# Kernel tuning notes

Measured on AMD Instinct MI355X. Metric: run time of the kernel, lower is better.

The kernel has to match this reference:

```python
import jax, jax.numpy as jnp
import numpy as np

B, N, D = 2048, 64, 256
DH = D // 2  # theta/phi projection dim
EPS = 1e-5

def layer_norm(x, g, b):
    m = jnp.mean(x, axis=-1, keepdims=True)
    v = jnp.var(x, axis=-1, keepdims=True)
    return (x - m) * jax.lax.rsqrt(v + EPS) * g + b

def graph_conv(x, adj, th_w, ph_w, fc_w, fc_b):
    # static adjacency: softmax over rows, shared across batch
    A_static = jax.nn.softmax(adj, axis=-1)  # [N, N]
    q = jnp.einsum('bnd,hd->bnh', x, th_w)   # [B, N, DH]
    k = jnp.einsum('bnd,hd->bnh', x, ph_w)   # [B, N, DH]
    scores = jnp.einsum('bni,bmi->bnm', q, k) / jnp.sqrt(jnp.asarray(DH, x.dtype))
    A_hat = A_static[None] + jax.nn.softmax(scores, axis=-1)  # [B, N, N]
    agg = jnp.einsum('bnm,bmd->bnd', A_hat, x)
    return jnp.einsum('bnd,od->bno', agg, fc_w) + fc_b

def setup_inputs() -> dict:
    key = jax.random.key(0)
    ks = jax.random.split(key, 12)
    eye = jnp.eye(N, dtype=jnp.float32)
    s = 1.0 / np.sqrt(D)
    return {
        'graph':  jax.random.normal(ks[0], (B, N, D), jnp.float32),
        'ln_in_g': jnp.ones((D,), jnp.float32), 'ln_in_b': jnp.zeros((D,), jnp.float32),
        'adj0':  eye + 0.01 * jax.random.normal(ks[1], (N, N), jnp.float32),
        'th0':   jax.random.uniform(ks[2], (DH, D), jnp.float32, -s, s),
        'ph0':   jax.random.uniform(ks[3], (DH, D), jnp.float32, -s, s),
        'fcw0':  jax.random.uniform(ks[4], (D, D), jnp.float32, -s, s),
        'fcb0':  jax.random.uniform(ks[5], (D,), jnp.float32, -s, s),
        'ln0_g': jnp.ones((D,), jnp.float32), 'ln0_b': jnp.zeros((D,), jnp.float32),
        'adj1':  eye + 0.01 * jax.random.normal(ks[6], (N, N), jnp.float32),
        'th1':   jax.random.uniform(ks[7], (DH, D), jnp.float32, -s, s),
        'ph1':   jax.random.uniform(ks[8], (DH, D), jnp.float32, -s, s),
        'fcw1':  jax.random.uniform(ks[9], (D, D), jnp.float32, -s, s),
        'fcb1':  jax.random.uniform(ks[10], (D,), jnp.float32, -s, s),
    }

def reference(graph, ln_in_g, ln_in_b, adj0, th0, ph0, fcw0, fcb0,
              ln0_g, ln0_b, adj1, th1, ph1, fcw1, fcb1):
    x = layer_norm(graph, ln_in_g, ln_in_b)
    x = graph_conv(x, adj0, th0, ph0, fcw0, fcb0)
    x = layer_norm(x, ln0_g, ln0_b)
    x = jnp.where(x >= 0, x, 0.1 * x)  # LeakyReLU(0.1); dropout is identity in eval
    x = graph_conv(x, adj1, th1, ph1, fcw1, fcb1)
    return x
```

## Files before the change

kernel.cpp:

```cpp
#include <hip/hip_runtime.h>

typedef __bf16 bf16x8 __attribute__((ext_vector_type(8)));
typedef __bf16 bf16x4 __attribute__((ext_vector_type(4)));
typedef float  f32x4  __attribute__((ext_vector_type(4)));

constexpr int WS_AS0 = 0;
constexpr int WS_AS1 = 4096;
constexpr int WS_MT0 = 8192;
constexpr int WS_MT1 = 73728;
constexpr int WS_FC0 = 139264;
constexpr int WS_FC1 = 204800;

static __device__ __forceinline__ f32x4 mfma16(bf16x8 a, bf16x8 b, f32x4 c) {
    return __builtin_amdgcn_mfma_f32_16x16x32_bf16(a, b, c, 0, 0, 0);
}

__global__ void prep_all(const float* __restrict__ adj0, const float* __restrict__ adj1,
                         const float* __restrict__ th0,  const float* __restrict__ ph0,
                         const float* __restrict__ th1,  const float* __restrict__ ph1,
                         const float* __restrict__ fc0,  const float* __restrict__ fc1,
                         __bf16* __restrict__ wsb) {
    const int blk = blockIdx.x, tid = threadIdx.x;
    if (blk < 32) {
        const int w = tid >> 6, lane = tid & 63;
        const int row = blk * 4 + w;
        const int layer = row >> 6, r = row & 63;
        const float* a = (layer ? adj1 : adj0) + r * 64;
        const float v = a[lane];
        float mx = v;
        #pragma unroll
        for (int m = 1; m < 64; m <<= 1) mx = fmaxf(mx, __shfl_xor(mx, m));
        float e = __expf(v - mx), sum = e;
        #pragma unroll
        for (int m = 1; m < 64; m <<= 1) sum += __shfl_xor(sum, m);
        wsb[(layer ? WS_AS1 : WS_AS0) + r * 64 + lane] = (__bf16)(e / sum);
    } else if (blk < 544) {
        const int e = (blk - 32) & 255, layer = (blk - 32) >> 8, d = tid;
        const float* th = layer ? th1 : th0;
        const float* ph = layer ? ph1 : ph0;
        float s = 0.f;
        #pragma unroll 8
        for (int h = 0; h < 128; ++h) s += ph[h * 256 + e] * th[h * 256 + d];
        wsb[(layer ? WS_MT1 : WS_MT0) + e * 256 + d] = (__bf16)(s * 0.088388347648318447f);
    } else {
        const int i = (blk - 544) * 512 + tid * 2;
        if (i < 65536) {
            wsb[WS_FC0 + i]     = (__bf16)fc0[i];
            wsb[WS_FC0 + i + 1] = (__bf16)fc0[i + 1];
        } else {
            wsb[WS_FC1 + i - 65536] = (__bf16)fc1[i - 65536];
            wsb[WS_FC1 + i - 65535] = (__bf16)fc1[i - 65535];
        }
    }
}

__global__ __launch_bounds__(512, 4) void fused_gcn(
    const float* __restrict__ graph,
    const float* __restrict__ ln_in_g, const float* __restrict__ ln_in_b,
    const __bf16* __restrict__ wsb,
    const float* __restrict__ fcb0, const float* __restrict__ ln0_g,
    const float* __restrict__ ln0_b, const float* __restrict__ fcb1,
    float* __restrict__ outp)
{
    constexpr int XN_S = 264;
    constexpr int ZT_S = 72;
    constexpr int AH_S = 72;

    __shared__ __align__(16) __bf16 sXn[64 * XN_S];
    __shared__ __align__(16) __bf16 sR1[256 * ZT_S];
    __shared__ __align__(16) __bf16 sAh[64 * AH_S];
    __shared__ float sRed[128];

    const int tid = threadIdx.x;
    const int w = tid >> 6, lane = tid & 63;
    const int l15 = lane & 15, qd = lane >> 4;
    const int b = blockIdx.x;

    {
        if (tid < 128) sRed[tid] = 0.f;
        const int r = tid >> 3, ci = (tid & 7) * 32;
        const float* gp = graph + (size_t)b * 16384 + r * 256 + ci;
        f32x4 v[8];
        float s = 0.f, s2 = 0.f;
        #pragma unroll
        for (int j = 0; j < 8; ++j) {
            v[j] = *(const f32x4*)(gp + j * 4);
            #pragma unroll
            for (int e = 0; e < 4; ++e) { s += v[j][e]; s2 += v[j][e] * v[j][e]; }
        }
        #pragma unroll
        for (int m = 1; m <= 4; m <<= 1) { s += __shfl_xor(s, m); s2 += __shfl_xor(s2, m); }
        const float mean = s * (1.f / 256.f);
        const float var  = s2 * (1.f / 256.f) - mean * mean;
        const float rstd = rsqrtf(var + 1e-5f);
        #pragma unroll
        for (int j = 0; j < 8; ++j) {
            f32x4 gg = *(const f32x4*)(ln_in_g + ci + j * 4);
            f32x4 bb = *(const f32x4*)(ln_in_b + ci + j * 4);
            bf16x4 pk;
            #pragma unroll
            for (int e = 0; e < 4; ++e)
                pk[e] = (__bf16)((v[j][e] - mean) * rstd * gg[e] + bb[e]);
            *(bf16x4*)&sXn[r * XN_S + ci + j * 4] = pk;
        }
    }
    __syncthreads();

    #pragma unroll 1
    for (int layer = 0; layer < 2; ++layer) {
        const __bf16* As  = wsb + (layer ? WS_AS1 : WS_AS0);
        const __bf16* mtw = wsb + (layer ? WS_MT1 : WS_MT0);
        const __bf16* fcw = wsb + (layer ? WS_FC1 : WS_FC0);
        const float*  fcb = layer ? fcb1 : fcb0;

        {
            {
                const int r = tid >> 3, c8 = (tid & 7) * 8;
                *(bf16x8*)&sAh[r * AH_S + c8] = *(const bf16x8*)(As + r * 64 + c8);
            }
            #pragma unroll
            for (int jm = 0; jm < 2; ++jm) {
                bf16x8 amt[8];
                #pragma unroll
                for (int kk = 0; kk < 8; ++kk)
                    amt[kk] = *(const bf16x8*)(mtw + ((w * 2 + jm) * 16 + l15) * 256 + kk * 32 + qd * 8);
                f32x4 tacc[4];
                #pragma unroll
                for (int nt = 0; nt < 4; ++nt) tacc[nt] = (f32x4){0.f, 0.f, 0.f, 0.f};
                #pragma unroll
                for (int kk = 0; kk < 8; ++kk)
                    #pragma unroll
                    for (int nt = 0; nt < 4; ++nt) {
                        bf16x8 bx = *(const bf16x8*)&sXn[(nt * 16 + l15) * XN_S + kk * 32 + qd * 8];
                        tacc[nt] = mfma16(amt[kk], bx, tacc[nt]);
                    }
                #pragma unroll
                for (int nt = 0; nt < 4; ++nt) {
                    bf16x4 pk;
                    #pragma unroll
                    for (int r = 0; r < 4; ++r) pk[r] = (__bf16)tacc[nt][r];
                    *(bf16x4*)&sR1[(nt * 16 + l15) * XN_S + (w * 2 + jm) * 16 + qd * 4] = pk;
                }
            }
        }
        __syncthreads();

        if (w < 4) {
            const int mb = w * 16;
            bf16x8 at[8];
            #pragma unroll
            for (int kk = 0; kk < 8; ++kk)
                at[kk] = *(const bf16x8*)&sR1[(mb + l15) * XN_S + kk * 32 + qd * 8];
            f32x4 sc[4];
            #pragma unroll
            for (int nt = 0; nt < 4; ++nt) sc[nt] = (f32x4){0.f, 0.f, 0.f, 0.f};
            #pragma unroll
            for (int nt = 0; nt < 4; ++nt)
                #pragma unroll
                for (int kk = 0; kk < 8; ++kk) {
                    bf16x8 bx = *(const bf16x8*)&sXn[(nt * 16 + l15) * XN_S + kk * 32 + qd * 8];
                    sc[nt] = mfma16(at[kk], bx, sc[nt]);
                }
            #pragma unroll
            for (int r = 0; r < 4; ++r) {
                float v[4];
                #pragma unroll
                for (int nt = 0; nt < 4; ++nt) v[nt] = sc[nt][r];
                float mx = fmaxf(fmaxf(v[0], v[1]), fmaxf(v[2], v[3]));
                #pragma unroll
                for (int m = 1; m <= 8; m <<= 1) mx = fmaxf(mx, __shfl_xor(mx, m));
                float e[4], sum = 0.f;
                #pragma unroll
                for (int nt = 0; nt < 4; ++nt) { e[nt] = __expf(v[nt] - mx); sum += e[nt]; }
                #pragma unroll
                for (int m = 1; m <= 8; m <<= 1) sum += __shfl_xor(sum, m);
                const float inv = 1.f / sum;
                const int row = mb + qd * 4 + r;
                #pragma unroll
                for (int nt = 0; nt < 4; ++nt) {
                    const int col = nt * 16 + l15;
                    const float as = (float)sAh[row * AH_S + col];
                    sAh[row * AH_S + col] = (__bf16)(e[nt] * inv + as);
                }
            }
        }
        __syncthreads();

        {
            #pragma unroll
            for (int jm = 0; jm < 2; ++jm) {
                const int o = w * 32 + jm * 16 + l15;
                bf16x8 bfc[8];
                #pragma unroll
                for (int kk = 0; kk < 8; ++kk)
                    bfc[kk] = *(const bf16x8*)(fcw + o * 256 + kk * 32 + qd * 8);
                f32x4 zacc[4];
                #pragma unroll
                for (int m = 0; m < 4; ++m) zacc[m] = (f32x4){0.f, 0.f, 0.f, 0.f};
                #pragma unroll
                for (int kk = 0; kk < 8; ++kk)
                    #pragma unroll
                    for (int m = 0; m < 4; ++m) {
                        bf16x8 ax = *(const bf16x8*)&sXn[(m * 16 + l15) * XN_S + kk * 32 + qd * 8];
                        zacc[m] = mfma16(ax, bfc[kk], zacc[m]);
                    }
                #pragma unroll
                for (int m = 0; m < 4; ++m) {
                    bf16x4 pk;
                    #pragma unroll
                    for (int r = 0; r < 4; ++r) pk[r] = (__bf16)zacc[m][r];
                    *(bf16x4*)&sR1[o * ZT_S + m * 16 + qd * 4] = pk;
                }
            }
        }
        __syncthreads();

        {
            const int mb = (w & 3) * 16, ng = w >> 2;
            bf16x8 aa[2];
            #pragma unroll
            for (int kk = 0; kk < 2; ++kk)
                aa[kk] = *(const bf16x8*)&sAh[(mb + l15) * AH_S + kk * 32 + qd * 8];
            f32x4 oacc[8];
            #pragma unroll
            for (int j = 0; j < 8; ++j) {
                const int o = ng * 128 + j * 16 + l15;
                f32x4 acc = {0.f, 0.f, 0.f, 0.f};
                #pragma unroll
                for (int kk = 0; kk < 2; ++kk) {
                    bf16x8 bb = *(const bf16x8*)&sR1[o * ZT_S + kk * 32 + qd * 8];
                    acc = mfma16(aa[kk], bb, acc);
                }
                const float bias = fcb[o];
                #pragma unroll
                for (int r = 0; r < 4; ++r) acc[r] += bias;
                oacc[j] = acc;
            }

            if (layer == 0) {
                #pragma unroll
                for (int r = 0; r < 4; ++r) {
                    float s = 0.f, s2 = 0.f;
                    #pragma unroll
                    for (int j = 0; j < 8; ++j) { const float vv = oacc[j][r]; s += vv; s2 += vv * vv; }
                    #pragma unroll
                    for (int m = 1; m <= 8; m <<= 1) { s += __shfl_xor(s, m); s2 += __shfl_xor(s2, m); }
                    if (l15 == 0) {
                        const int row = mb + qd * 4 + r;
                        atomicAdd(&sRed[row], s);
                        atomicAdd(&sRed[64 + row], s2);
                    }
                }
                __syncthreads();
                float mean4[4], rstd4[4];
                #pragma unroll
                for (int r = 0; r < 4; ++r) {
                    const int row = mb + qd * 4 + r;
                    const float mean = sRed[row] * (1.f / 256.f);
                    const float var  = sRed[64 + row] * (1.f / 256.f) - mean * mean;
                    mean4[r] = mean;
                    rstd4[r] = rsqrtf(var + 1e-5f);
                }
                #pragma unroll
                for (int j = 0; j < 8; ++j) {
                    const int o = ng * 128 + j * 16 + l15;
                    const float g = ln0_g[o], bb = ln0_b[o];
                    #pragma unroll
                    for (int r = 0; r < 4; ++r) {
                        float y = (oacc[j][r] - mean4[r]) * rstd4[r] * g + bb;
                        y = (y >= 0.f) ? y : 0.1f * y;
                        sXn[(mb + qd * 4 + r) * XN_S + o] = (__bf16)y;
                    }
                }
                __syncthreads();
            } else {
                float* op = outp + (size_t)b * 16384;
                #pragma unroll
                for (int j = 0; j < 8; ++j) {
                    const int o = ng * 128 + j * 16 + l15;
                    #pragma unroll
                    for (int r = 0; r < 4; ++r)
                        op[(mb + qd * 4 + r) * 256 + o] = oacc[j][r];
                }
            }
        }
    }
}

extern "C" void kernel_launch(void* const* d_in, const int* in_sizes, int n_in,
                              void* d_out, int out_size, void* d_ws, size_t ws_size,
                              hipStream_t stream) {
    const float* graph   = (const float*)d_in[0];
    const float* ln_in_g = (const float*)d_in[1];
    const float* ln_in_b = (const float*)d_in[2];
    const float* adj0    = (const float*)d_in[3];
    const float* th0     = (const float*)d_in[4];
    const float* ph0     = (const float*)d_in[5];
    const float* fcw0    = (const float*)d_in[6];
    const float* fcb0    = (const float*)d_in[7];
    const float* ln0_g   = (const float*)d_in[8];
    const float* ln0_b   = (const float*)d_in[9];
    const float* adj1    = (const float*)d_in[10];
    const float* th1     = (const float*)d_in[11];
    const float* ph1     = (const float*)d_in[12];
    const float* fcw1    = (const float*)d_in[13];
    const float* fcb1    = (const float*)d_in[14];
    __bf16* wsb = (__bf16*)d_ws;

    prep_all<<<800, 256, 0, stream>>>(adj0, adj1, th0, ph0, th1, ph1, fcw0, fcw1, wsb);
    fused_gcn<<<2048, 512, 0, stream>>>(graph, ln_in_g, ln_in_b, wsb,
                                        fcb0, ln0_g, ln0_b, fcb1, (float*)d_out);
}
```

Measured before the change: 404.4 us.

## Persistent blocks over four batches with graph prefetch and fused theta/fc GEMM

The grid shrinks from 2048 to 512 blocks, and each block loops over four batch elements. The next batch's graph rows are prefetched into registers during the second layer, so the global load overlaps compute. The theta projection and fc projection GEMMs are merged into one pass over sXn. The fc result is held in registers and written to shared memory after the softmax phase, which removes one barrier phase. The costs are higher register pressure (the prefetch buffer plus zpk) and fewer blocks, which may leave compute units underused on a 256-CU GPU.

```diff
diff --git a/kernel.cpp b/kernel.cpp
--- a/kernel.cpp
+++ b/kernel.cpp
@@ -74,213 +74,219 @@
     const int tid = threadIdx.x;
     const int w = tid >> 6, lane = tid & 63;
     const int l15 = lane & 15, qd = lane >> 4;
-    const int b = blockIdx.x;
-
+    const int r8 = tid >> 3, ci8 = (tid & 7) * 32;
+
+    f32x4 gv[8];
     {
-        if (tid < 128) sRed[tid] = 0.f;
-        const int r = tid >> 3, ci = (tid & 7) * 32;
-        const float* gp = graph + (size_t)b * 16384 + r * 256 + ci;
-        f32x4 v[8];
-        float s = 0.f, s2 = 0.f;
+        const float* gp = graph + (size_t)blockIdx.x * 16384 + r8 * 256 + ci8;
         #pragma unroll
-        for (int j = 0; j < 8; ++j) {
-            v[j] = *(const f32x4*)(gp + j * 4);
+        for (int j = 0; j < 8; ++j) gv[j] = *(const f32x4*)(gp + j * 4);
+    }
+
+    #pragma unroll 1
+    for (int it = 0; it < 4; ++it) {
+        const int b = blockIdx.x + it * 512;
+
+        {
+            if (tid < 128) sRed[tid] = 0.f;
+            float s = 0.f, s2 = 0.f;
             #pragma unroll
-            for (int e = 0; e < 4; ++e) { s += v[j][e]; s2 += v[j][e] * v[j][e]; }
-        }
-        #pragma unroll
-        for (int m = 1; m <= 4; m <<= 1) { s += __shfl_xor(s, m); s2 += __shfl_xor(s2, m); }
-        const float mean = s * (1.f / 256.f);
-        const float var  = s2 * (1.f / 256.f) - mean * mean;
-        const float rstd = rsqrtf(var + 1e-5f);
-        #pragma unroll
-        for (int j = 0; j < 8; ++j) {
-            f32x4 gg = *(const f32x4*)(ln_in_g + ci + j * 4);
-            f32x4 bb = *(const f32x4*)(ln_in_b + ci + j * 4);
-            bf16x4 pk;
+            for (int j = 0; j < 8; ++j)
+                #pragma unroll
+                for (int e = 0; e < 4; ++e) { s += gv[j][e]; s2 += gv[j][e] * gv[j][e]; }
             #pragma unroll
-            for (int e = 0; e < 4; ++e)
-                pk[e] = (__bf16)((v[j][e] - mean) * rstd * gg[e] + bb[e]);
-            *(bf16x4*)&sXn[r * XN_S + ci + j * 4] = pk;
-        }
-    }
-    __syncthreads();
-
-    #pragma unroll 1
-    for (int layer = 0; layer < 2; ++layer) {
-        const __bf16* As  = wsb + (layer ? WS_AS1 : WS_AS0);
-        const __bf16* mtw = wsb + (layer ? WS_MT1 : WS_MT0);
-        const __bf16* fcw = wsb + (layer ? WS_FC1 : WS_FC0);
-        const float*  fcb = layer ? fcb1 : fcb0;
-
-        {
-            {
-                const int r = tid >> 3, c8 = (tid & 7) * 8;
-                *(bf16x8*)&sAh[r * AH_S + c8] = *(const bf16x8*)(As + r * 64 + c8);
-            }
+            for (int m = 1; m <= 4; m <<= 1) { s += __shfl_xor(s, m); s2 += __shfl_xor(s2, m); }
+            const float mean = s * (1.f / 256.f);
+            const float var  = s2 * (1.f / 256.f) - mean * mean;
+            const float rstd = rsqrtf(var + 1e-5f);
             #pragma unroll
-            for (int jm = 0; jm < 2; ++jm) {
-                bf16x8 amt[8];
-                #pragma unroll
-                for (int kk = 0; kk < 8; ++kk)
-                    amt[kk] = *(const bf16x8*)(mtw + ((w * 2 + jm) * 16 + l15) * 256 + kk * 32 + qd * 8);
-                f32x4 tacc[4];
-                #pragma unroll
-                for (int nt = 0; nt < 4; ++nt) tacc[nt] = (f32x4){0.f, 0.f, 0.f, 0.f};
-                #pragma unroll
-                for (int kk = 0; kk < 8; ++kk)
-                    #pragma unroll
-                    for (int nt = 0; nt < 4; ++nt) {
-                        bf16x8 bx = *(const bf16x8*)&sXn[(nt * 16 + l15) * XN_S + kk * 32 + qd * 8];
-                        tacc[nt] = mfma16(amt[kk], bx, tacc[nt]);
-                    }
-                #pragma unroll
-                for (int nt = 0; nt < 4; ++nt) {
-                    bf16x4 pk;
-                    #pragma unroll
-                    for (int r = 0; r < 4; ++r) pk[r] = (__bf16)tacc[nt][r];
-                    *(bf16x4*)&sR1[(nt * 16 + l15) * XN_S + (w * 2 + jm) * 16 + qd * 4] = pk;
-                }
+            for (int j = 0; j < 8; ++j) {
+                f32x4 gg = *(const f32x4*)(ln_in_g + ci8 + j * 4);
+                f32x4 bb = *(const f32x4*)(ln_in_b + ci8 + j * 4);
+                bf16x4 pk;
+                #pragma unroll
+                for (int e = 0; e < 4; ++e)
+                    pk[e] = (__bf16)((gv[j][e] - mean) * rstd * gg[e] + bb[e]);
+                *(bf16x4*)&sXn[r8 * XN_S + ci8 + j * 4] = pk;
             }
         }
         __syncthreads();
 
-        if (w < 4) {
-            const int mb = w * 16;
-            bf16x8 at[8];
-            #pragma unroll
-            for (int kk = 0; kk < 8; ++kk)
-                at[kk] = *(const bf16x8*)&sR1[(mb + l15) * XN_S + kk * 32 + qd * 8];
-            f32x4 sc[4];
-            #pragma unroll
-            for (int nt = 0; nt < 4; ++nt) sc[nt] = (f32x4){0.f, 0.f, 0.f, 0.f};
-            #pragma unroll
-            for (int nt = 0; nt < 4; ++nt)
-                #pragma unroll
-                for (int kk = 0; kk < 8; ++kk) {
-                    bf16x8 bx = *(const bf16x8*)&sXn[(nt * 16 + l15) * XN_S + kk * 32 + qd * 8];
-                    sc[nt] = mfma16(at[kk], bx, sc[nt]);
-                }
-            #pragma unroll
-            for (int r = 0; r < 4; ++r) {
-                float v[4];
-                #pragma unroll
-                for (int nt = 0; nt < 4; ++nt) v[nt] = sc[nt][r];
-                float mx = fmaxf(fmaxf(v[0], v[1]), fmaxf(v[2], v[3]));
-                #pragma unroll
-                for (int m = 1; m <= 8; m <<= 1) mx = fmaxf(mx, __shfl_xor(mx, m));
-                float e[4], sum = 0.f;
-                #pragma unroll
-                for (int nt = 0; nt < 4; ++nt) { e[nt] = __expf(v[nt] - mx); sum += e[nt]; }
-                #pragma unroll
-                for (int m = 1; m <= 8; m <<= 1) sum += __shfl_xor(sum, m);
-                const float inv = 1.f / sum;
-                const int row = mb + qd * 4 + r;
-                #pragma unroll
-                for (int nt = 0; nt < 4; ++nt) {
-                    const int col = nt * 16 + l15;
-                    const float as = (float)sAh[row * AH_S + col];
-                    sAh[row * AH_S + col] = (__bf16)(e[nt] * inv + as);
-                }
-            }
-        }
-        __syncthreads();
-
-        {
-            #pragma unroll
-            for (int jm = 0; jm < 2; ++jm) {
-                const int o = w * 32 + jm * 16 + l15;
-                bf16x8 bfc[8];
+        #pragma unroll 1
+        for (int layer = 0; layer < 2; ++layer) {
+            const __bf16* As  = wsb + (layer ? WS_AS1 : WS_AS0);
+            const __bf16* mtw = wsb + (layer ? WS_MT1 : WS_MT0);
+            const __bf16* fcw = wsb + (layer ? WS_FC1 : WS_FC0);
+            const float*  fcb = layer ? fcb1 : fcb0;
+
+            bf16x4 zpk[4][2];
+
+            {
+                {
+                    const int rr = tid >> 3, c8 = (tid & 7) * 8;
+                    *(bf16x8*)&sAh[rr * AH_S + c8] = *(const bf16x8*)(As + rr * 64 + c8);
+                }
+                #pragma unroll
+                for (int jm = 0; jm < 2; ++jm) {
+                    const int row = w * 32 + jm * 16 + l15;
+                    f32x4 tacc[4], zacc[4];
+                    #pragma unroll
+                    for (int i = 0; i < 4; ++i) {
+                        tacc[i] = (f32x4){0.f, 0.f, 0.f, 0.f};
+                        zacc[i] = (f32x4){0.f, 0.f, 0.f, 0.f};
+                    }
+                    #pragma unroll
+                    for (int kk = 0; kk < 8; ++kk) {
+                        const int co = kk * 32 + qd * 8;
+                        bf16x8 amt = *(const bf16x8*)(mtw + row * 256 + co);
+                        bf16x8 afc = *(const bf16x8*)(fcw + row * 256 + co);
+                        #pragma unroll
+                        for (int nt = 0; nt < 4; ++nt) {
+                            bf16x8 bx = *(const bf16x8*)&sXn[(nt * 16 + l15) * XN_S + co];
+                            tacc[nt] = mfma16(amt, bx, tacc[nt]);
+                            zacc[nt] = mfma16(bx, afc, zacc[nt]);
+                        }
+                    }
+                    #pragma unroll
+                    for (int nt = 0; nt < 4; ++nt) {
+                        bf16x4 pk;
+                        #pragma unroll
+                        for (int r = 0; r < 4; ++r) pk[r] = (__bf16)tacc[nt][r];
+                        *(bf16x4*)&sR1[(nt * 16 + l15) * XN_S + (w * 2 + jm) * 16 + qd * 4] = pk;
+                    }
+                    #pragma unroll
+                    for (int nt = 0; nt < 4; ++nt)
+                        #pragma unroll
+                        for (int r = 0; r < 4; ++r)
+                            zpk[nt][jm][r] = (__bf16)zacc[nt][r];
+                }
+            }
+            __syncthreads();
+
+            if (w < 4) {
+                const int mb = w * 16;
+                bf16x8 at[8];
                 #pragma unroll
                 for (int kk = 0; kk < 8; ++kk)
-                    bfc[kk] = *(const bf16x8*)(fcw + o * 256 + kk * 32 + qd * 8);
-                f32x4 zacc[4];
-                #pragma unroll
-                for (int m = 0; m < 4; ++m) zacc[m] = (f32x4){0.f, 0.f, 0.f, 0.f};
-                #pragma unroll
-                for (int kk = 0; kk < 8; ++kk)
-                    #pragma unroll
-                    for (int m = 0; m < 4; ++m) {
-                        bf16x8 ax = *(const bf16x8*)&sXn[(m * 16 + l15) * XN_S + kk * 32 + qd * 8];
-                        zacc[m] = mfma16(ax, bfc[kk], zacc[m]);
-                    }
-                #pragma unroll
-                for (int m = 0; m < 4; ++m) {
-                    bf16x4 pk;
-                    #pragma unroll
-                    for (int r = 0; r < 4; ++r) pk[r] = (__bf16)zacc[m][r];
-                    *(bf16x4*)&sR1[o * ZT_S + m * 16 + qd * 4] = pk;
-                }
-            }
-        }
-        __syncthreads();
-
-        {
-            const int mb = (w & 3) * 16, ng = w >> 2;
-            bf16x8 aa[2];
-            #pragma unroll
-            for (int kk = 0; kk < 2; ++kk)
-                aa[kk] = *(const bf16x8*)&sAh[(mb + l15) * AH_S + kk * 32 + qd * 8];
-            f32x4 oacc[8];
-            #pragma unroll
-            for (int j = 0; j < 8; ++j) {
-                const int o = ng * 128 + j * 16 + l15;
-                f32x4 acc = {0.f, 0.f, 0.f, 0.f};
-                #pragma unroll
-                for (int kk = 0; kk < 2; ++kk) {
-                    bf16x8 bb = *(const bf16x8*)&sR1[o * ZT_S + kk * 32 + qd * 8];
-                    acc = mfma16(aa[kk], bb, acc);
-                }
-                const float bias = fcb[o];
-                #pragma unroll
-                for (int r = 0; r < 4; ++r) acc[r] += bias;
-                oacc[j] = acc;
-            }
-
-            if (layer == 0) {
+                    at[kk] = *(const bf16x8*)&sR1[(mb + l15) * XN_S + kk * 32 + qd * 8];
+                f32x4 sc[4];
+                #pragma unroll
+                for (int nt = 0; nt < 4; ++nt) sc[nt] = (f32x4){0.f, 0.f, 0.f, 0.f};
+                #pragma unroll
+                for (int nt = 0; nt < 4; ++nt)
+                    #pragma unroll
+                    for (int kk = 0; kk < 8; ++kk) {
+                        bf16x8 bx = *(const bf16x8*)&sXn[(nt * 16 + l15) * XN_S + kk * 32 + qd * 8];
+                        sc[nt] = mfma16(at[kk], bx, sc[nt]);
+                    }
                 #pragma unroll
                 for (int r = 0; r < 4; ++r) {
-                    float s = 0.f, s2 = 0.f;
-                    #pragma unroll
-                    for (int j = 0; j < 8; ++j) { const float vv = oacc[j][r]; s += vv; s2 += vv * vv; }
-                    #pragma unroll
-                    for (int m = 1; m <= 8; m <<= 1) { s += __shfl_xor(s, m); s2 += __shfl_xor(s2, m); }
-                    if (l15 == 0) {
-                        const int row = mb + qd * 4 + r;
-                        atomicAdd(&sRed[row], s);
-                        atomicAdd(&sRed[64 + row], s2);
-                    }
-                }
-                __syncthreads();
-                float mean4[4], rstd4[4];
-                #pragma unroll
-                for (int r = 0; r < 4; ++r) {
+                    float v[4];
+                    #pragma unroll
+                    for (int nt = 0; nt < 4; ++nt) v[nt] = sc[nt][r];
+                    float mx = fmaxf(fmaxf(v[0], v[1]), fmaxf(v[2], v[3]));
+                    #pragma unroll
+                    for (int m = 1; m <= 8; m <<= 1) mx = fmaxf(mx, __shfl_xor(mx, m));
+                    float e[4], sum = 0.f;
+                    #pragma unroll
+                    for (int nt = 0; nt < 4; ++nt) { e[nt] = __expf(v[nt] - mx); sum += e[nt]; }
+                    #pragma unroll
+                    for (int m = 1; m <= 8; m <<= 1) sum += __shfl_xor(sum, m);
+                    const float inv = 1.f / sum;
                     const int row = mb + qd * 4 + r;
-                    const float mean = sRed[row] * (1.f / 256.f);
-                    const float var  = sRed[64 + row] * (1.f / 256.f) - mean * mean;
-                    mean4[r] = mean;
-                    rstd4[r] = rsqrtf(var + 1e-5f);
-                }
+                    #pragma unroll
+                    for (int nt = 0; nt < 4; ++nt) {
+                        const int col = nt * 16 + l15;
+                        const float as = (float)sAh[row * AH_S + col];
+                        sAh[row * AH_S + col] = (__bf16)(e[nt] * inv + as);
+                    }
+                }
+            }
+            __syncthreads();
+
+            {
+                #pragma unroll
+                for (int jm = 0; jm < 2; ++jm) {
+                    const int o = w * 32 + jm * 16 + l15;
+                    #pragma unroll
+                    for (int nt = 0; nt < 4; ++nt)
+                        *(bf16x4*)&sR1[o * ZT_S + nt * 16 + qd * 4] = zpk[nt][jm];
+                }
+            }
+            if (layer == 1 && it < 3) {
+                const float* gp = graph + (size_t)(b + 512) * 16384 + r8 * 256 + ci8;
+                #pragma unroll
+                for (int j = 0; j < 8; ++j) gv[j] = *(const f32x4*)(gp + j * 4);
+            }
+            __syncthreads();
+
+            {
+                const int mb = (w & 3) * 16, ng = w >> 2;
+                bf16x8 aa[2];
+                #pragma unroll
+                for (int kk = 0; kk < 2; ++kk)
+                    aa[kk] = *(const bf16x8*)&sAh[(mb + l15) * AH_S + kk * 32 + qd * 8];
+                f32x4 oacc[8];
                 #pragma unroll
                 for (int j = 0; j < 8; ++j) {
                     const int o = ng * 128 + j * 16 + l15;
-                    const float g = ln0_g[o], bb = ln0_b[o];
+                    f32x4 acc = {0.f, 0.f, 0.f, 0.f};
+                    #pragma unroll
+                    for (int kk = 0; kk < 2; ++kk) {
+                        bf16x8 bb = *(const bf16x8*)&sR1[o * ZT_S + kk * 32 + qd * 8];
+                        acc = mfma16(aa[kk], bb, acc);
+                    }
+                    const float bias = fcb[o];
+                    #pragma unroll
+                    for (int r = 0; r < 4; ++r) acc[r] += bias;
+                    oacc[j] = acc;
+                }
+
+                if (layer == 0) {
                     #pragma unroll
                     for (int r = 0; r < 4; ++r) {
-                        float y = (oacc[j][r] - mean4[r]) * rstd4[r] * g + bb;
-                        y = (y >= 0.f) ? y : 0.1f * y;
-                        sXn[(mb + qd * 4 + r) * XN_S + o] = (__bf16)y;
-                    }
-                }
-                __syncthreads();
-            } else {
-                float* op = outp + (size_t)b * 16384;
-                #pragma unroll
-                for (int j = 0; j < 8; ++j) {
-                    const int o = ng * 128 + j * 16 + l15;
-                    #pragma unroll
-                    for (int r = 0; r < 4; ++r)
-                        op[(mb + qd * 4 + r) * 256 + o] = oacc[j][r];
+                        float s = 0.f, s2 = 0.f;
+                        #pragma unroll
+                        for (int j = 0; j < 8; ++j) { const float vv = oacc[j][r]; s += vv; s2 += vv * vv; }
+                        #pragma unroll
+                        for (int m = 1; m <= 8; m <<= 1) { s += __shfl_xor(s, m); s2 += __shfl_xor(s2, m); }
+                        if (l15 == 0) {
+                            const int row = mb + qd * 4 + r;
+                            atomicAdd(&sRed[row], s);
+                            atomicAdd(&sRed[64 + row], s2);
+                        }
+                    }
+                    __syncthreads();
+                    float mean4[4], rstd4[4];
+                    #pragma unroll
+                    for (int r = 0; r < 4; ++r) {
+                        const int row = mb + qd * 4 + r;
+                        const float mean = sRed[row] * (1.f / 256.f);
+                        const float var  = sRed[64 + row] * (1.f / 256.f) - mean * mean;
+                        mean4[r] = mean;
+                        rstd4[r] = rsqrtf(var + 1e-5f);
+                    }
+                    #pragma unroll
+                    for (int j = 0; j < 8; ++j) {
+                        const int o = ng * 128 + j * 16 + l15;
+                        const float g = ln0_g[o], bb = ln0_b[o];
+                        #pragma unroll
+                        for (int r = 0; r < 4; ++r) {
+                            float y = (oacc[j][r] - mean4[r]) * rstd4[r] * g + bb;
+                            y = (y >= 0.f) ? y : 0.1f * y;
+                            sXn[(mb + qd * 4 + r) * XN_S + o] = (__bf16)y;
+                        }
+                    }
+                    __syncthreads();
+                } else {
+                    float* op = outp + (size_t)b * 16384;
+                    #pragma unroll
+                    for (int j = 0; j < 8; ++j) {
+                        const int o = ng * 128 + j * 16 + l15;
+                        #pragma unroll
+                        for (int r = 0; r < 4; ++r)
+                            op[(mb + qd * 4 + r) * 256 + o] = oacc[j][r];
+                    }
                 }
             }
         }
@@ -308,6 +314,6 @@
     __bf16* wsb = (__bf16*)d_ws;
 
     prep_all<<<800, 256, 0, stream>>>(adj0, adj1, th0, ph0, th1, ph1, fcw0, fcw1, wsb);
-    fused_gcn<<<2048, 512, 0, stream>>>(graph, ln_in_g, ln_in_b, wsb,
-                                        fcb0, ln0_g, ln0_b, fcb1, (float*)d_out);
+    fused_gcn<<<512, 512, 0, stream>>>(graph, ln_in_g, ln_in_b, wsb,
+                                       fcb0, ln0_g, ln0_b, fcb1, (float*)d_out);
 }
```

After: 481.9 us. 1.19x slower.
